# Optimization experiments

Hardware: AMD Instinct MI355X
Metric: run time of the kernel (lower is better)

Reference implementation:

```python
import jax, jax.numpy as jnp
import numpy as np

SEARCH_RANGE = 4  # matches init_kwargs


def setup_inputs() -> dict:
    key = jax.random.key(0)
    k1, k2 = jax.random.split(key)
    shape = (8, 256, 64, 128)  # [B, C, H, W]
    feature1 = jax.random.normal(k1, shape, dtype=jnp.float32)
    feature2 = jax.random.normal(k2, shape, dtype=jnp.float32)
    return {"feature1": feature1, "feature2": feature2}


def reference(feature1, feature2):
    R = SEARCH_RANGE
    b, c, h, w = feature1.shape
    # zero-pad feature2 spatially by R on each side
    f2p = jnp.pad(feature2, ((0, 0), (0, 0), (R, R), (R, R)))
    D = 2 * R + 1
    # shift offsets in the same order as the original nested loop (idx outer, jdx inner)
    offsets = jnp.stack(
        jnp.meshgrid(jnp.arange(D), jnp.arange(D), indexing="ij"), axis=-1
    ).reshape(-1, 2)  # [81, 2]

    def corr_one(ij):
        win = jax.lax.dynamic_slice(f2p, (0, 0, ij[0], ij[1]), (b, c, h, w))
        return jnp.sum(feature1 * win, axis=1)  # [B, H, W]

    dots = jax.vmap(corr_one)(offsets)  # [81, B, H, W]
    return jnp.transpose(dots, (1, 0, 2, 3))  # [B, 81, H, W]
```

## Files before the change

### kernel.cpp

```cpp
#include <hip/hip_runtime.h>
#include <cstdint>

typedef __attribute__((ext_vector_type(8))) short short8;
typedef __attribute__((ext_vector_type(4))) float floatx4;
typedef __attribute__((ext_vector_type(2))) unsigned int uintx2;
typedef __attribute__((ext_vector_type(4))) unsigned int uintx4;

#define CS 18
#define A_WORDS (8 * 32 * CS)
#define B_WORDS (16 * 48 * CS)

__device__ __forceinline__ uint32_t pack2(float a, float b) {
    uint32_t ua = __builtin_bit_cast(uint32_t, a);
    uint32_t ub = __builtin_bit_cast(uint32_t, b);
    ua = (ua + 0x7FFFu + ((ua >> 16) & 1u)) >> 16;
    ub = (ub + 0x7FFFu + ((ub >> 16) & 1u)) >> 16;
    return ua | (ub << 16);
}

__device__ __forceinline__ short8 frag_ld(const uint32_t* p) {
    uintx2 lo = *(const uintx2*)p;
    uintx2 hi = *(const uintx2*)(p + 2);
    uintx4 v = {lo.x, lo.y, hi.x, hi.y};
    return __builtin_bit_cast(short8, v);
}

__global__ __launch_bounds__(512, 2)
void corr_kernel(const float* __restrict__ f1, const float* __restrict__ f2,
                 float* __restrict__ out) {
    __shared__ uint32_t ldsA[2 * A_WORDS];
    __shared__ uint32_t ldsB[2 * B_WORDS];

    const int tid  = threadIdx.x;
    const int lane = tid & 63;
    const int wh   = tid >> 6;
    const int n15  = lane & 15;
    const int q    = lane >> 4;

    const int bid = blockIdx.x;
    const int b  = bid & 7;
    const int ht = (bid >> 3) & 7;
    const int wt = bid >> 6;

    const int w0 = wt * 32;
    const int h0 = ht * 8;
    const int h  = h0 + wh;

    const float* f1b = f1 + (size_t)b * 256 * 8192;
    const float* f2b = f2 + (size_t)b * 256 * 8192;

    const float* aPtr[2];
    int aOff[2];
#pragma unroll
    for (int s = 0; s < 2; ++s) {
        int t = tid + 512 * s;
        int w4 = t & 7, kp = (t >> 3) & 15, row = t >> 7;
        aPtr[s] = f1b + (size_t)(2 * kp) * 8192 + (h0 + row) * 128 + (w0 + 4 * w4);
        aOff[s] = (row * 32 + 4 * w4) * CS + kp;
    }
    const float* bPtr[6];
    int bOff[6];
    uint32_t bMask[6];
#pragma unroll
    for (int s = 0; s < 6; ++s) {
        int t = tid + 512 * s;
        int w4 = t % 12;
        int r2 = t / 12;
        int kp = r2 & 15, row = r2 >> 4;
        int gh = h0 - 4 + row;
        int gw = w0 - 4 + 4 * w4;
        bool inb = ((unsigned)gh < 64u) && ((unsigned)gw < 128u);
        bPtr[s]  = inb ? (f2b + (size_t)(2 * kp) * 8192 + gh * 128 + gw) : f2b;
        bOff[s]  = (row * 48 + 4 * w4) * CS + kp;
        bMask[s] = inb ? 0xFFFFFFFFu : 0u;
    }

    floatx4 acc[9][4];
#pragma unroll
    for (int di = 0; di < 9; ++di)
#pragma unroll
        for (int t = 0; t < 4; ++t)
            acc[di][t] = (floatx4){0.f, 0.f, 0.f, 0.f};

    floatx4 rA[2][2], rB[6][2];
    uint32_t pkA[8], pkB[24];

    auto issue = [&]() {
#pragma unroll
        for (int s = 0; s < 2; ++s) {
            rA[s][0] = *(const floatx4*)aPtr[s];
            rA[s][1] = *(const floatx4*)(aPtr[s] + 8192);
            aPtr[s] += 32 * 8192;
        }
#pragma unroll
        for (int s = 0; s < 6; ++s) {
            rB[s][0] = *(const floatx4*)bPtr[s];
            rB[s][1] = *(const floatx4*)(bPtr[s] + 8192);
            bPtr[s] += 32 * 8192;
        }
    };
    auto packall = [&]() {
#pragma unroll
        for (int s = 0; s < 2; ++s)
#pragma unroll
            for (int i = 0; i < 4; ++i)
                pkA[4 * s + i] = pack2(rA[s][0][i], rA[s][1][i]);
#pragma unroll
        for (int s = 0; s < 6; ++s)
#pragma unroll
            for (int i = 0; i < 4; ++i)
                pkB[4 * s + i] = pack2(rB[s][0][i], rB[s][1][i]) & bMask[s];
    };

    issue();
    packall();

    for (int ch = 0; ch < 8; ++ch) {
        uint32_t* bufA = ldsA + (ch & 1) * A_WORDS;
        uint32_t* bufB = ldsB + (ch & 1) * B_WORDS;

#pragma unroll
        for (int s = 0; s < 2; ++s)
#pragma unroll
            for (int i = 0; i < 4; ++i)
                bufA[aOff[s] + i * CS] = pkA[4 * s + i];
#pragma unroll
        for (int s = 0; s < 6; ++s)
#pragma unroll
            for (int i = 0; i < 4; ++i)
                bufB[bOff[s] + i * CS] = pkB[4 * s + i];

        if (ch < 7) issue();
        __syncthreads();

        const uint32_t* pa = bufA + (wh * 32 + n15) * CS + 4 * q;
        short8 a0 = frag_ld(pa);
        short8 a1 = frag_ld(pa + 16 * CS);
#pragma unroll
        for (int di = 0; di < 9; ++di) {
            const uint32_t* pb = bufB + ((wh + di) * 48 + n15) * CS + 4 * q;
            short8 b0 = frag_ld(pb);
            short8 b1 = frag_ld(pb + 16 * CS);
            short8 b2 = frag_ld(pb + 32 * CS);
            acc[di][0] = __builtin_amdgcn_mfma_f32_16x16x32_bf16(a0, b0, acc[di][0], 0, 0, 0);
            acc[di][1] = __builtin_amdgcn_mfma_f32_16x16x32_bf16(a0, b1, acc[di][1], 0, 0, 0);
            acc[di][2] = __builtin_amdgcn_mfma_f32_16x16x32_bf16(a1, b1, acc[di][2], 0, 0, 0);
            acc[di][3] = __builtin_amdgcn_mfma_f32_16x16x32_bf16(a1, b2, acc[di][3], 0, 0, 0);
        }
        if (ch < 7) packall();
    }

    const int At[4] = {0, 0, 1, 1};
    const int Bt[4] = {0, 1, 1, 2};
#pragma unroll
    for (int di = 0; di < 9; ++di) {
#pragma unroll
        for (int t = 0; t < 4; ++t) {
#pragma unroll
            for (int r = 0; r < 4; ++r) {
                int mp = 4 * q + r;
                int dj = (Bt[t] - At[t]) * 16 + n15 - mp;
                if (dj >= 0 && dj <= 8) {
                    int w = w0 + At[t] * 16 + mp;
                    size_t idx = (((size_t)b * 81 + (size_t)(di * 9 + dj)) * 64 + h) * 128 + w;
                    out[idx] = acc[di][t][r];
                }
            }
        }
    }
}

extern "C" void kernel_launch(void* const* d_in, const int* in_sizes, int n_in,
                              void* d_out, int out_size, void* d_ws, size_t ws_size,
                              hipStream_t stream) {
    const float* f1 = (const float*)d_in[0];
    const float* f2 = (const float*)d_in[1];
    float* out = (float*)d_out;
    corr_kernel<<<dim3(256), dim3(512), 0, stream>>>(f1, f2, out);
}
```

Measured before the change: 186.4 us.

## Split work across displacement rows and narrower width tiles for more blocks

Raises the grid from 256 to 1024 blocks by halving the width tile to 16 columns and splitting the 9 vertical displacement rows into two groups of 5 and 4 per block. The per-block LDS footprint and accumulator count shrink, and launch bounds are raised to allow 4 blocks per CU, to improve occupancy and fill more CUs. MFMA fragments are reorganised into overlapping 16-wide B tiles offset by 8, so some MFMA output is wasted and f1 plus the f2 halo are reloaded more often across blocks.

Result: no change. 187.8 us (+0.8%).

```diff
diff --git a/kernel.cpp b/kernel.cpp
--- a/kernel.cpp
+++ b/kernel.cpp
@@ -7,8 +7,9 @@
 typedef __attribute__((ext_vector_type(4))) unsigned int uintx4;
 
 #define CS 18
-#define A_WORDS (8 * 32 * CS)
-#define B_WORDS (16 * 48 * CS)
+#define A_WORDS (8 * 16 * CS)
+#define B_ROWS  13
+#define B_WORDS (B_ROWS * 24 * CS)
 
 __device__ __forceinline__ uint32_t pack2(float a, float b) {
     uint32_t ua = __builtin_bit_cast(uint32_t, a);
@@ -25,7 +26,7 @@
     return __builtin_bit_cast(short8, v);
 }
 
-__global__ __launch_bounds__(512, 2)
+__global__ __launch_bounds__(512, 4)
 void corr_kernel(const float* __restrict__ f1, const float* __restrict__ f2,
                  float* __restrict__ out) {
     __shared__ uint32_t ldsA[2 * A_WORDS];
@@ -37,76 +38,73 @@
     const int n15  = lane & 15;
     const int q    = lane >> 4;
 
-    const int bid = blockIdx.x;
-    const int b  = bid & 7;
-    const int ht = (bid >> 3) & 7;
-    const int wt = bid >> 6;
+    const int bid    = blockIdx.x;
+    const int b      = bid & 7;
+    const int dihalf = (bid >> 3) & 1;
+    const int ht     = (bid >> 4) & 7;
+    const int wt     = bid >> 7;
 
-    const int w0 = wt * 32;
+    const int w0 = wt * 16;
     const int h0 = ht * 8;
     const int h  = h0 + wh;
+
+    const int diN    = dihalf ? 4 : 5;
+    const int diBase = dihalf * 5;
+    const int ghBase = dihalf ? (h0 + 1) : (h0 - 4);
 
     const float* f1b = f1 + (size_t)b * 256 * 8192;
     const float* f2b = f2 + (size_t)b * 256 * 8192;
 
-    const float* aPtr[2];
-    int aOff[2];
+    const int aw4 = tid & 3, akp = (tid >> 2) & 15, arow = tid >> 6;
+    int aOffG = (2 * akp) * 8192 + (h0 + arow) * 128 + (w0 + 4 * aw4);
+    const int aLds = (arow * 16 + 4 * aw4) * CS + akp;
+
+    int bOffG[3];
+    int bLds[3];
+    uint32_t bMask[3];
 #pragma unroll
-    for (int s = 0; s < 2; ++s) {
+    for (int s = 0; s < 3; ++s) {
         int t = tid + 512 * s;
-        int w4 = t & 7, kp = (t >> 3) & 15, row = t >> 7;
-        aPtr[s] = f1b + (size_t)(2 * kp) * 8192 + (h0 + row) * 128 + (w0 + 4 * w4);
-        aOff[s] = (row * 32 + 4 * w4) * CS + kp;
-    }
-    const float* bPtr[6];
-    int bOff[6];
-    uint32_t bMask[6];
-#pragma unroll
-    for (int s = 0; s < 6; ++s) {
-        int t = tid + 512 * s;
-        int w4 = t % 12;
-        int r2 = t / 12;
+        int w4 = t % 6;
+        int r2 = t / 6;
         int kp = r2 & 15, row = r2 >> 4;
-        int gh = h0 - 4 + row;
+        int gh = ghBase + row;
         int gw = w0 - 4 + 4 * w4;
-        bool inb = ((unsigned)gh < 64u) && ((unsigned)gw < 128u);
-        bPtr[s]  = inb ? (f2b + (size_t)(2 * kp) * 8192 + gh * 128 + gw) : f2b;
-        bOff[s]  = (row * 48 + 4 * w4) * CS + kp;
+        bool live = (t < 1152);
+        bool inb  = live && ((unsigned)gh < 64u) && ((unsigned)gw < 128u);
+        bOffG[s] = inb ? ((2 * kp) * 8192 + gh * 128 + gw) : 0;
+        bLds[s]  = live ? ((row * 24 + 4 * w4) * CS + kp)
+                        : ((12 * 24 + (tid & 7)) * CS);
         bMask[s] = inb ? 0xFFFFFFFFu : 0u;
     }
 
-    floatx4 acc[9][4];
+    floatx4 acc[5][2];
 #pragma unroll
-    for (int di = 0; di < 9; ++di)
+    for (int dl = 0; dl < 5; ++dl)
 #pragma unroll
-        for (int t = 0; t < 4; ++t)
-            acc[di][t] = (floatx4){0.f, 0.f, 0.f, 0.f};
+        for (int t = 0; t < 2; ++t)
+            acc[dl][t] = (floatx4){0.f, 0.f, 0.f, 0.f};
 
-    floatx4 rA[2][2], rB[6][2];
-    uint32_t pkA[8], pkB[24];
+    floatx4 rA[2], rB[3][2];
+    uint32_t pkA[4], pkB[12];
 
     auto issue = [&]() {
+        rA[0] = *(const floatx4*)(f1b + aOffG);
+        rA[1] = *(const floatx4*)(f1b + aOffG + 8192);
+        aOffG += 32 * 8192;
 #pragma unroll
-        for (int s = 0; s < 2; ++s) {
-            rA[s][0] = *(const floatx4*)aPtr[s];
-            rA[s][1] = *(const floatx4*)(aPtr[s] + 8192);
-            aPtr[s] += 32 * 8192;
-        }
-#pragma unroll
-        for (int s = 0; s < 6; ++s) {
-            rB[s][0] = *(const floatx4*)bPtr[s];
-            rB[s][1] = *(const floatx4*)(bPtr[s] + 8192);
-            bPtr[s] += 32 * 8192;
+        for (int s = 0; s < 3; ++s) {
+            rB[s][0] = *(const floatx4*)(f2b + bOffG[s]);
+            rB[s][1] = *(const floatx4*)(f2b + bOffG[s] + 8192);
+            bOffG[s] += 32 * 8192;
         }
     };
     auto packall = [&]() {
 #pragma unroll
-        for (int s = 0; s < 2; ++s)
+        for (int i = 0; i < 4; ++i)
+            pkA[i] = pack2(rA[0][i], rA[1][i]);
 #pragma unroll
-            for (int i = 0; i < 4; ++i)
-                pkA[4 * s + i] = pack2(rA[s][0][i], rA[s][1][i]);
-#pragma unroll
-        for (int s = 0; s < 6; ++s)
+        for (int s = 0; s < 3; ++s)
 #pragma unroll
             for (int i = 0; i < 4; ++i)
                 pkB[4 * s + i] = pack2(rB[s][0][i], rB[s][1][i]) & bMask[s];
@@ -120,50 +118,47 @@
         uint32_t* bufB = ldsB + (ch & 1) * B_WORDS;
 
 #pragma unroll
-        for (int s = 0; s < 2; ++s)
+        for (int i = 0; i < 4; ++i)
+            bufA[aLds + i * CS] = pkA[i];
+#pragma unroll
+        for (int s = 0; s < 3; ++s)
 #pragma unroll
             for (int i = 0; i < 4; ++i)
-                bufA[aOff[s] + i * CS] = pkA[4 * s + i];
-#pragma unroll
-        for (int s = 0; s < 6; ++s)
-#pragma unroll
-            for (int i = 0; i < 4; ++i)
-                bufB[bOff[s] + i * CS] = pkB[4 * s + i];
+                bufB[bLds[s] + i * CS] = pkB[4 * s + i];
 
         if (ch < 7) issue();
         __syncthreads();
 
-        const uint32_t* pa = bufA + (wh * 32 + n15) * CS + 4 * q;
+        const uint32_t* pa = bufA + (wh * 16 + n15) * CS + 4 * q;
         short8 a0 = frag_ld(pa);
-        short8 a1 = frag_ld(pa + 16 * CS);
+        const uint32_t* pb = bufB + (wh * 24 + n15) * CS + 4 * q;
 #pragma unroll
-        for (int di = 0; di < 9; ++di) {
-            const uint32_t* pb = bufB + ((wh + di) * 48 + n15) * CS + 4 * q;
-            short8 b0 = frag_ld(pb);
-            short8 b1 = frag_ld(pb + 16 * CS);
-            short8 b2 = frag_ld(pb + 32 * CS);
-            acc[di][0] = __builtin_amdgcn_mfma_f32_16x16x32_bf16(a0, b0, acc[di][0], 0, 0, 0);
-            acc[di][1] = __builtin_amdgcn_mfma_f32_16x16x32_bf16(a0, b1, acc[di][1], 0, 0, 0);
-            acc[di][2] = __builtin_amdgcn_mfma_f32_16x16x32_bf16(a1, b1, acc[di][2], 0, 0, 0);
-            acc[di][3] = __builtin_amdgcn_mfma_f32_16x16x32_bf16(a1, b2, acc[di][3], 0, 0, 0);
+        for (int dl = 0; dl < 5; ++dl) {
+            if (dl < diN) {
+                const uint32_t* p = pb + dl * (24 * CS);
+                short8 b0 = frag_ld(p);
+                short8 b1 = frag_ld(p + 8 * CS);
+                acc[dl][0] = __builtin_amdgcn_mfma_f32_16x16x32_bf16(a0, b0, acc[dl][0], 0, 0, 0);
+                acc[dl][1] = __builtin_amdgcn_mfma_f32_16x16x32_bf16(a0, b1, acc[dl][1], 0, 0, 0);
+            }
         }
         if (ch < 7) packall();
     }
 
-    const int At[4] = {0, 0, 1, 1};
-    const int Bt[4] = {0, 1, 1, 2};
+    const size_t base = ((size_t)b * 81) * 8192 + (size_t)h * 128 + w0;
 #pragma unroll
-    for (int di = 0; di < 9; ++di) {
+    for (int dl = 0; dl < 5; ++dl) {
+        if (dl < diN) {
+            const int dio = diBase + dl;
 #pragma unroll
-        for (int t = 0; t < 4; ++t) {
+            for (int t = 0; t < 2; ++t) {
 #pragma unroll
-            for (int r = 0; r < 4; ++r) {
-                int mp = 4 * q + r;
-                int dj = (Bt[t] - At[t]) * 16 + n15 - mp;
-                if (dj >= 0 && dj <= 8) {
-                    int w = w0 + At[t] * 16 + mp;
-                    size_t idx = (((size_t)b * 81 + (size_t)(di * 9 + dj)) * 64 + h) * 128 + w;
-                    out[idx] = acc[di][t][r];
+                for (int r = 0; r < 4; ++r) {
+                    int mp = 4 * q + r;
+                    int dj = t * 8 + n15 - mp;
+                    if (dj >= 0 && dj <= 8 && (t == 0 || n15 >= 8)) {
+                        out[base + (size_t)(dio * 9 + dj) * 8192 + mp] = acc[dl][t][r];
+                    }
                 }
             }
         }
@@ -176,5 +171,5 @@
     const float* f1 = (const float*)d_in[0];
     const float* f2 = (const float*)d_in[1];
     float* out = (float*)d_out;
-    corr_kernel<<<dim3(256), dim3(512), 0, stream>>>(f1, f2, out);
+    corr_kernel<<<dim3(1024), dim3(512), 0, stream>>>(f1, f2, out);
 }
```
